# Kernel optimization log

Measured on AMD Instinct MI355X. Metric: run time of the kernel, lower is better.

The kernel has to match this reference:

```python
import jax, jax.numpy as jnp
import numpy as np
import math

TOPK = 13
NUM_CLASSES = 80
ALPHA = 1.0
BETA = 6.0
EPS = 1e-9


def ciou_xyxy(box1, box2, eps=1e-7):
    """CIoU between xyxy boxes; box1/box2 broadcastable [..., 4]. Returns [..., 1]."""
    b1x1, b1y1, b1x2, b1y2 = jnp.split(box1, 4, axis=-1)
    b2x1, b2y1, b2x2, b2y2 = jnp.split(box2, 4, axis=-1)
    w1, h1 = b1x2 - b1x1, b1y2 - b1y1 + eps
    w2, h2 = b2x2 - b2x1, b2y2 - b2y1 + eps
    inter = (jnp.minimum(b1x2, b2x2) - jnp.maximum(b1x1, b2x1)).clip(0) * \
            (jnp.minimum(b1y2, b2y2) - jnp.maximum(b1y1, b2y1)).clip(0)
    union = w1 * h1 + w2 * h2 - inter + eps
    iou = inter / union
    cw = jnp.maximum(b1x2, b2x2) - jnp.minimum(b1x1, b2x1)
    ch = jnp.maximum(b1y2, b2y2) - jnp.minimum(b1y1, b2y1)
    c2 = cw ** 2 + ch ** 2 + eps
    rho2 = ((b2x1 + b2x2 - b1x1 - b1x2) ** 2 + (b2y1 + b2y2 - b1y1 - b1y2) ** 2) / 4
    v = (4.0 / math.pi ** 2) * (jnp.arctan(w2 / h2) - jnp.arctan(w1 / h1)) ** 2
    alpha = jax.lax.stop_gradient(v / (v - iou + (1 + eps)))  # torch.no_grad block
    return iou - (rho2 / c2 + v * alpha)


def setup_inputs() -> dict:
    key = jax.random.key(0)
    ks = jax.random.split(key, 8)
    bs, M = 16, 64
    # YOLOv8 anchor grid: strides 8/16/32 on a 640x640 image -> 8400 points
    pts = []
    for s, n in ((8, 80), (16, 40), (32, 20)):
        xs = (np.arange(n, dtype=np.float32) + 0.5) * s
        gx, gy = np.meshgrid(xs, xs)
        pts.append(np.stack([gx.ravel(), gy.ravel()], -1))
    anc_points = jnp.asarray(np.concatenate(pts, 0), jnp.float32)  # (8400, 2)
    A = anc_points.shape[0]
    pd_scores = jax.random.uniform(ks[0], (bs, A, NUM_CLASSES), jnp.float32)
    c = jax.random.uniform(ks[1], (bs, A, 2), jnp.float32) * 640.0
    wh = jax.random.uniform(ks[2], (bs, A, 2), jnp.float32) * 120.0 + 8.0
    pd_bboxes = jnp.concatenate([c - wh / 2, c + wh / 2], -1)  # xyxy
    gc = jax.random.uniform(ks[3], (bs, M, 2), jnp.float32) * 560.0 + 40.0
    gwh = jax.random.uniform(ks[4], (bs, M, 2), jnp.float32) * 200.0 + 20.0
    gt_bboxes = jnp.concatenate([gc - gwh / 2, gc + gwh / 2], -1)
    gt_labels = jax.random.randint(ks[5], (bs, M, 1), 0, NUM_CLASSES, dtype=jnp.int32)
    mask_gt = (jax.random.uniform(ks[6], (bs, M, 1)) > 0.25).astype(jnp.float32)
    return {"pd_scores": pd_scores, "pd_bboxes": pd_bboxes, "anc_points": anc_points,
            "gt_labels": gt_labels, "gt_bboxes": gt_bboxes, "mask_gt": mask_gt}


def _assign(pd_scores, pd_bboxes, anc_points, gt_labels, gt_bboxes, mask_gt):
    bs, A, nc = pd_scores.shape
    M = gt_bboxes.shape[1]
    dt = pd_scores.dtype

    # ---- select_candidates_in_gts: anchors inside gt boxes -> (b, M, A) ----
    lt = gt_bboxes[:, :, None, :2]            # (b, M, 1, 2)
    rb = gt_bboxes[:, :, None, 2:]
    xy = anc_points[None, None]               # (1, 1, A, 2)
    deltas = jnp.concatenate([xy - lt, rb - xy], axis=-1)  # (b, M, A, 4)
    mask_in_gts = (deltas.min(-1) > EPS).astype(dt)        # (b, M, A)

    # ---- get_box_metrics ----
    bidx = jnp.arange(bs)[:, None]                         # (b, 1)
    labels = gt_labels[..., 0].astype(jnp.int32)           # (b, M)
    bbox_scores = pd_scores[bidx, :, labels]               # (b, M, A)
    overlaps = ciou_xyxy(gt_bboxes[:, :, None, :], pd_bboxes[:, None, :, :])
    overlaps = overlaps[..., 0].clip(0)                    # (b, M, A)
    align_metric = bbox_scores ** ALPHA * overlaps ** BETA

    # ---- select_topk_candidates (scatter-add instead of one_hot over 8400) ----
    metrics = align_metric * mask_in_gts
    _, topk_idxs = jax.lax.top_k(metrics, TOPK)            # (b, M, topk)
    valid = mask_gt > 0                                    # (b, M, 1) bool
    topk_idxs = jnp.where(valid, topk_idxs, 0)
    counts = jnp.zeros((bs, M, A), dt).at[
        jnp.arange(bs)[:, None, None], jnp.arange(M)[None, :, None], topk_idxs
    ].add(1.0)
    mask_topk = jnp.where(counts > 1, jnp.zeros((), dt), counts)
    mask_pos = mask_topk * mask_in_gts * mask_gt           # (b, M, A)

    # ---- select_highest_overlaps (unconditional; identity when no conflicts) ----
    fg_mask = mask_pos.sum(-2)                             # (b, A)
    mask_multi = fg_mask[:, None, :] > 1                   # (b, 1, A)
    max_idx = overlaps.argmax(1)                           # (b, A)
    is_max = jnp.swapaxes(jax.nn.one_hot(max_idx, M, dtype=dt), 1, 2)  # (b, M, A)
    mask_pos = jnp.where(mask_multi, is_max, mask_pos)
    fg_mask = mask_pos.sum(-2)
    target_gt_idx = mask_pos.argmax(-2)                    # (b, A)

    # ---- get_targets ----
    flat_idx = target_gt_idx + bidx * M                    # (b, A) into b*M
    target_labels = jnp.clip(gt_labels.reshape(-1)[flat_idx], 0)   # (b, A)
    target_bboxes = gt_bboxes.reshape(-1, 4)[flat_idx]             # (b, A, 4)
    target_scores = jax.nn.one_hot(target_labels, NUM_CLASSES, dtype=dt)
    target_scores = jnp.where(fg_mask[..., None] > 0, target_scores, jnp.zeros((), dt))

    # ---- normalize scores by aligned metric ----
    align_metric = align_metric * mask_pos
    pos_align = align_metric.max(-1, keepdims=True)        # (b, M, 1)
    pos_overlaps = (overlaps * mask_pos).max(-1, keepdims=True)
    norm = (align_metric * pos_overlaps / (pos_align + EPS)).max(-2)[..., None]  # (b, A, 1)
    target_scores = target_scores * norm

    return target_labels, target_bboxes, target_scores, fg_mask.astype(bool), target_gt_idx


def reference(pd_scores, pd_bboxes, anc_points, gt_labels, gt_bboxes, mask_gt):
    return _assign(pd_scores, pd_bboxes, anc_points, gt_labels, gt_bboxes, mask_gt)
```

## Files before the change

kernel.cpp:

```cpp
#include <hip/hip_runtime.h>

#define A_TOT 8400
#define NCLS  80
#define MGT   64
#define TK    13
#define EPS7  1e-7f
#define EPS9  1e-9f
#define INV_PI2 0.4052847345693511f

__device__ __forceinline__ float ciou_clip(
    float gx1, float gy1, float gx2, float gy2, float ga, float area1,
    float px1, float py1, float px2, float py2, float pa)
{
  float w2 = px2 - px1, h2 = py2 - py1 + EPS7;
  float iw = fmaxf(fminf(gx2, px2) - fmaxf(gx1, px1), 0.f);
  float ih = fmaxf(fminf(gy2, py2) - fmaxf(gy1, py1), 0.f);
  float inter = iw * ih;
  float uni = area1 + w2 * h2 - inter + EPS7;
  float iou = inter / uni;
  float cw = fmaxf(gx2, px2) - fminf(gx1, px1);
  float ch = fmaxf(gy2, py2) - fminf(gy1, py1);
  float c2 = cw * cw + ch * ch + EPS7;
  float dx = px1 + px2 - gx1 - gx2;
  float dy = py1 + py2 - gy1 - gy2;
  float rho2 = (dx * dx + dy * dy) * 0.25f;
  float dd = pa - ga;
  float v = INV_PI2 * dd * dd;
  float alpha = v / (v - iou + (1.f + EPS7));
  float c = iou - (rho2 / c2 + v * alpha);
  return fmaxf(c, 0.f);
}

__device__ __forceinline__ unsigned long long wmax64(unsigned long long k) {
#pragma unroll
  for (int s = 32; s > 0; s >>= 1) {
    unsigned long long o = __shfl_xor(k, s, 64);
    k = (o > k) ? o : k;
  }
  return k;
}

__global__ void k_pre(const float* __restrict__ pd_bboxes,
                      const float* __restrict__ gt_bboxes,
                      float* __restrict__ patan, float* __restrict__ gatan,
                      int na, int nm)
{
  int t = blockIdx.x * 256 + threadIdx.x;
  if (t < na) {
    float4 bx = ((const float4*)pd_bboxes)[t];
    patan[t] = atanf((bx.z - bx.x) / (bx.w - bx.y + EPS7));
  } else if (t < na + nm) {
    int r = t - na;
    float4 bx = ((const float4*)gt_bboxes)[r];
    gatan[r] = atanf((bx.z - bx.x) / (bx.w - bx.y + EPS7));
  }
}

__global__ __launch_bounds__(64)
void k_topk(const float* __restrict__ pd_scores,
            const float* __restrict__ pd_bboxes,
            const float* __restrict__ anc,
            const int* __restrict__ gt_labels,
            const float* __restrict__ gt_bboxes,
            const float* __restrict__ mask_gt,
            const float* __restrict__ patan,
            const float* __restrict__ gatan,
            unsigned long long* __restrict__ mask64)
{
  int row = blockIdx.x;
  if (mask_gt[row] <= 0.f) return;
  int b = row >> 6;
  int m = row & 63;
  int lane = threadIdx.x;

  float4 g = ((const float4*)gt_bboxes)[row];
  float ga = gatan[row];
  float area1 = (g.z - g.x) * (g.w - g.y + EPS7);
  int label = gt_labels[row];
  const float*  ps   = pd_scores + (size_t)b * A_TOT * NCLS + label;
  const float4* pb   = (const float4*)(pd_bboxes + (size_t)b * A_TOT * 4);
  const float*  pat  = patan + (size_t)b * A_TOT;
  const float2* anc2 = (const float2*)anc;

  unsigned long long l[TK];
#pragma unroll
  for (int k = 0; k < TK; ++k) l[k] = 0ULL;

  auto insert = [&](unsigned long long key) {
    if (key > l[TK - 1]) {
#pragma unroll
      for (int j = TK - 1; j > 0; --j) {
        unsigned long long prev = l[j - 1];
        l[j] = (key > prev) ? prev : ((key > l[j]) ? key : l[j]);
      }
      l[0] = (key > l[0]) ? key : l[0];
    }
  };
  auto metric_key = [&](int a, float ax, float ay) -> unsigned long long {
    float dmin = fminf(fminf(ax - g.x, ay - g.y), fminf(g.z - ax, g.w - ay));
    unsigned long long key = (unsigned long long)(~(unsigned)a);
    if (dmin > EPS9) {
      float4 p = pb[a];
      float ov = ciou_clip(g.x, g.y, g.z, g.w, ga, area1, p.x, p.y, p.z, p.w, pat[a]);
      float o2 = ov * ov;
      float metric = ps[(size_t)a * NCLS] * (o2 * o2 * o2);
      key |= ((unsigned long long)__float_as_uint(metric)) << 32;
    }
    return key;
  };

  {
    float2 an = anc2[lane];
    insert(metric_key(lane, an.x, an.y));
  }

  const int   ns[3] = {80, 40, 20};
  const float ss[3] = {8.f, 16.f, 32.f};
  const int   bb[3] = {0, 6400, 8000};
#pragma unroll
  for (int sc = 0; sc < 3; ++sc) {
    int n = ns[sc]; float s = ss[sc]; int base = bb[sc];
    float inv_s = 1.f / s;
    int xlo = max(0,     (int)floorf(g.x * inv_s - 0.5f));
    int xhi = min(n - 1, (int)ceilf (g.z * inv_s - 0.5f));
    int ylo = max(0,     (int)floorf(g.y * inv_s - 0.5f));
    int yhi = min(n - 1, (int)ceilf (g.w * inv_s - 0.5f));
    int nx = xhi - xlo + 1, ny = yhi - ylo + 1;
    if (nx <= 0 || ny <= 0) continue;
    int tot = nx * ny;
    float invnx = 1.f / (float)nx;
    for (int r = lane; r < tot; r += 64) {
      int q  = (int)floorf(((float)r + 0.5f) * invnx);
      int ix = xlo + (r - q * nx);
      int iy = ylo + q;
      int a = base + iy * n + ix;
      if (a < 64) continue;
      float ax = ((float)ix + 0.5f) * s;
      float ay = ((float)iy + 0.5f) * s;
      float dmin = fminf(fminf(ax - g.x, ay - g.y), fminf(g.z - ax, g.w - ay));
      if (dmin > EPS9) {
        float4 p = pb[a];
        float ov = ciou_clip(g.x, g.y, g.z, g.w, ga, area1, p.x, p.y, p.z, p.w, pat[a]);
        float o2 = ov * ov;
        float metric = ps[(size_t)a * NCLS] * (o2 * o2 * o2);
        insert((((unsigned long long)__float_as_uint(metric)) << 32) |
               (unsigned long long)(~(unsigned)a));
      }
    }
  }

  unsigned long long res = 0ULL;
#pragma unroll
  for (int r = 0; r < TK; ++r) {
    unsigned long long w = wmax64(l[0]);
    if (lane == r) res = w;
    if (l[0] == w) {
#pragma unroll
      for (int j = 0; j < TK - 1; ++j) l[j] = l[j + 1];
      l[TK - 1] = 0ULL;
    }
  }

  if (lane < TK) {
    unsigned a = ~(unsigned)res;
    float2 an = anc2[a];
    float dmin = fminf(fminf(an.x - g.x, an.y - g.y), fminf(g.z - an.x, g.w - an.y));
    if (dmin > EPS9)
      atomicOr(mask64 + (size_t)b * A_TOT + a, 1ULL << m);
  }
}

__global__ __launch_bounds__(256)
void k_resolve(const float* __restrict__ pd_scores,
               const float* __restrict__ pd_bboxes,
               const int* __restrict__ gt_labels,
               const float* __restrict__ gt_bboxes,
               const float* __restrict__ patan,
               const float* __restrict__ gatan,
               const unsigned long long* __restrict__ mask64,
               int* __restrict__ tgt_ws, float* __restrict__ am_ws,
               unsigned int* __restrict__ pos_al, unsigned int* __restrict__ pos_ov,
               int total)
{
  int t = blockIdx.x * 256 + threadIdx.x;
  bool valid = t < total;
  unsigned long long msk = valid ? mask64[t] : 0ULL;
  int pc = __popcll(msk);
  float4 p = make_float4(0.f, 0.f, 0.f, 0.f);
  float pa_own = 0.f;
  if (valid && pc >= 1) {
    p = ((const float4*)pd_bboxes)[t];
    pa_own = patan[t];
  }
  if (valid && pc == 0) tgt_ws[t] = -1;
  if (valid && pc == 1) {
    int b = t / A_TOT;
    int tgt = __ffsll(msk) - 1;
    int gi = b * MGT + tgt;
    float4 g = ((const float4*)gt_bboxes)[gi];
    float area1 = (g.z - g.x) * (g.w - g.y + EPS7);
    float ov = ciou_clip(g.x, g.y, g.z, g.w, gatan[gi], area1,
                         p.x, p.y, p.z, p.w, pa_own);
    int label = gt_labels[gi];
    float sc = pd_scores[(size_t)t * NCLS + label];
    float o2 = ov * ov;
    float am = sc * (o2 * o2 * o2);
    tgt_ws[t] = tgt; am_ws[t] = am;
    atomicMax(pos_al + gi, __float_as_uint(am));
    atomicMax(pos_ov + gi, __float_as_uint(ov));
  }
  unsigned long long mb = __ballot(valid && pc > 1);
  int lane = threadIdx.x & 63;
  while (mb) {
    int src = __ffsll(mb) - 1; mb &= mb - 1;
    int   tt  = __shfl(t, src);
    float px1 = __shfl(p.x, src), py1 = __shfl(p.y, src);
    float px2 = __shfl(p.z, src), py2 = __shfl(p.w, src);
    float pa  = __shfl(pa_own, src);
    int bb2 = tt / A_TOT;
    int gi = bb2 * MGT + lane;
    float4 g = ((const float4*)gt_bboxes)[gi];
    float area1 = (g.z - g.x) * (g.w - g.y + EPS7);
    float ov = ciou_clip(g.x, g.y, g.z, g.w, gatan[gi], area1,
                         px1, py1, px2, py2, pa);
    unsigned long long key =
        (((unsigned long long)__float_as_uint(ov)) << 6) | (unsigned)(63 - lane);
    unsigned long long w = wmax64(key);
    if (key == w) {
      int label = gt_labels[gi];
      float sc = pd_scores[(size_t)tt * NCLS + label];
      float o2 = ov * ov;
      float am = sc * (o2 * o2 * o2);
      tgt_ws[tt] = lane; am_ws[tt] = am;
      atomicMax(pos_al + gi, __float_as_uint(am));
      atomicMax(pos_ov + gi, __float_as_uint(ov));
    }
  }
}

__global__ __launch_bounds__(256)
void k_write(const int* __restrict__ tgt_ws, const float* __restrict__ am_ws,
             const unsigned int* __restrict__ pos_al,
             const unsigned int* __restrict__ pos_ov,
             const int* __restrict__ gt_labels, const float* __restrict__ gt_bboxes,
             float* __restrict__ out, int bs)
{
  __shared__ int   slab[256];
  __shared__ float snorm[256];
  int total = bs * A_TOT;
  int base = blockIdx.x * 256;
  int t = base + threadIdx.x;
  int nrows = total - base; if (nrows > 256) nrows = 256;
  size_t OFF_BOX = (size_t)total;
  size_t OFF_SCR = OFF_BOX + (size_t)total * 4;
  size_t OFF_FG  = OFF_SCR + (size_t)total * NCLS;
  size_t OFF_TGT = OFF_FG + (size_t)total;
  if (t < total) {
    int b = t / A_TOT;
    int tw = tgt_ws[t];
    bool fg = tw >= 0;
    int tgt = fg ? tw : 0;
    int gi = b * MGT + tgt;
    int lab = gt_labels[gi]; if (lab < 0) lab = 0;
    float4 box = ((const float4*)gt_bboxes)[gi];
    float nrm = 0.f;
    if (fg) {
      float pa_ = __uint_as_float(pos_al[gi]);
      float po  = __uint_as_float(pos_ov[gi]);
      nrm = am_ws[t] * po / (pa_ + EPS9);
    }
    out[t] = (float)lab;
    ((float4*)(out + OFF_BOX))[t] = box;
    out[OFF_FG + t]  = fg ? 1.f : 0.f;
    out[OFF_TGT + t] = (float)tgt;
    slab[threadIdx.x]  = lab;
    snorm[threadIdx.x] = nrm;
  }
  __syncthreads();
  float4* srow = (float4*)(out + OFF_SCR + (size_t)base * NCLS);
  int nvec = nrows * (NCLS / 4);
  for (int u = threadIdx.x; u < nvec; u += 256) {
    int i  = u / (NCLS / 4);
    int c0 = (u - i * (NCLS / 4)) * 4;
    int lb = slab[i]; float nv = snorm[i];
    float4 v;
    v.x = (lb == c0    ) ? nv : 0.f;
    v.y = (lb == c0 + 1) ? nv : 0.f;
    v.z = (lb == c0 + 2) ? nv : 0.f;
    v.w = (lb == c0 + 3) ? nv : 0.f;
    srow[u] = v;
  }
}

extern "C" void kernel_launch(void* const* d_in, const int* in_sizes, int n_in,
                              void* d_out, int out_size, void* d_ws, size_t ws_size,
                              hipStream_t stream)
{
  const float* pd_scores = (const float*)d_in[0];
  const float* pd_bboxes = (const float*)d_in[1];
  const float* anc       = (const float*)d_in[2];
  const int*   gt_labels = (const int*)d_in[3];
  const float* gt_bboxes = (const float*)d_in[4];
  const float* mask_gt   = (const float*)d_in[5];
  int bs = in_sizes[0] / (A_TOT * NCLS);
  int NA = bs * A_TOT, NM = bs * MGT;

  unsigned long long* mask64 = (unsigned long long*)d_ws;
  unsigned int* pos_al = (unsigned int*)(mask64 + NA);
  unsigned int* pos_ov = pos_al + NM;
  int*   tgt_ws = (int*)(pos_ov + NM);
  float* am_ws  = (float*)(tgt_ws + NA);
  float* patan  = am_ws + NA;
  float* gatan  = patan + NA;

  hipMemsetAsync(mask64, 0, (size_t)NA * 8 + (size_t)NM * 8, stream);

  k_pre<<<(NA + NM + 255) / 256, 256, 0, stream>>>(pd_bboxes, gt_bboxes,
                                                   patan, gatan, NA, NM);
  k_topk<<<NM, 64, 0, stream>>>(pd_scores, pd_bboxes, anc, gt_labels, gt_bboxes,
                                mask_gt, patan, gatan, mask64);
  k_resolve<<<(NA + 255) / 256, 256, 0, stream>>>(pd_scores, pd_bboxes, gt_labels,
                                                  gt_bboxes, patan, gatan, mask64,
                                                  tgt_ws, am_ws, pos_al, pos_ov, NA);
  k_write<<<(NA + 255) / 256, 256, 0, stream>>>(tgt_ws, am_ws, pos_al, pos_ov,
                                                gt_labels, gt_bboxes, (float*)d_out, bs);
}
```

Baseline: 132.7 us.

## Widen top-k blocks to four wavefronts and compute atan inline, dropping pre-pass

The per-GT top-k kernel now runs 256 threads (four wavefronts) instead of one. Each wavefront keeps its own per-lane top-13 lists, and the four candidate sets are merged through shared memory by the first wavefront. The separate atan precompute kernel is removed; aspect-ratio arctangents are computed inline where needed, saving one launch and its global traffic at the cost of extra transcendental work per evaluated anchor. The first 256 anchors are always inserted, which keeps the index-tiebreak semantics of the original.

```diff
diff --git a/kernel.cpp b/kernel.cpp
--- a/kernel.cpp
+++ b/kernel.cpp
@@ -4,6 +4,7 @@
 #define NCLS  80
 #define MGT   64
 #define TK    13
+#define NT    256
 #define EPS7  1e-7f
 #define EPS9  1e-9f
 #define INV_PI2 0.4052847345693511f
@@ -40,46 +41,27 @@
   return k;
 }
 
-__global__ void k_pre(const float* __restrict__ pd_bboxes,
-                      const float* __restrict__ gt_bboxes,
-                      float* __restrict__ patan, float* __restrict__ gatan,
-                      int na, int nm)
-{
-  int t = blockIdx.x * 256 + threadIdx.x;
-  if (t < na) {
-    float4 bx = ((const float4*)pd_bboxes)[t];
-    patan[t] = atanf((bx.z - bx.x) / (bx.w - bx.y + EPS7));
-  } else if (t < na + nm) {
-    int r = t - na;
-    float4 bx = ((const float4*)gt_bboxes)[r];
-    gatan[r] = atanf((bx.z - bx.x) / (bx.w - bx.y + EPS7));
-  }
-}
-
-__global__ __launch_bounds__(64)
+__global__ __launch_bounds__(NT)
 void k_topk(const float* __restrict__ pd_scores,
             const float* __restrict__ pd_bboxes,
             const float* __restrict__ anc,
             const int* __restrict__ gt_labels,
             const float* __restrict__ gt_bboxes,
             const float* __restrict__ mask_gt,
-            const float* __restrict__ patan,
-            const float* __restrict__ gatan,
             unsigned long long* __restrict__ mask64)
 {
   int row = blockIdx.x;
   if (mask_gt[row] <= 0.f) return;
   int b = row >> 6;
   int m = row & 63;
-  int lane = threadIdx.x;
+  int tid = threadIdx.x, lane = tid & 63, wid = tid >> 6;
 
   float4 g = ((const float4*)gt_bboxes)[row];
-  float ga = gatan[row];
+  float ga = atanf((g.z - g.x) / (g.w - g.y + EPS7));
   float area1 = (g.z - g.x) * (g.w - g.y + EPS7);
   int label = gt_labels[row];
   const float*  ps   = pd_scores + (size_t)b * A_TOT * NCLS + label;
   const float4* pb   = (const float4*)(pd_bboxes + (size_t)b * A_TOT * 4);
-  const float*  pat  = patan + (size_t)b * A_TOT;
   const float2* anc2 = (const float2*)anc;
 
   unsigned long long l[TK];
@@ -96,22 +78,23 @@
       l[0] = (key > l[0]) ? key : l[0];
     }
   };
-  auto metric_key = [&](int a, float ax, float ay) -> unsigned long long {
-    float dmin = fminf(fminf(ax - g.x, ay - g.y), fminf(g.z - ax, g.w - ay));
+  auto eval_inbox = [&](int a) -> unsigned long long {
+    float4 p = pb[a];
+    float pa = atanf((p.z - p.x) / (p.w - p.y + EPS7));
+    float ov = ciou_clip(g.x, g.y, g.z, g.w, ga, area1, p.x, p.y, p.z, p.w, pa);
+    float o2 = ov * ov;
+    float metric = ps[(size_t)a * NCLS] * (o2 * o2 * o2);
+    return (((unsigned long long)__float_as_uint(metric)) << 32) |
+           (unsigned long long)(~(unsigned)a);
+  };
+
+  {
+    int a = tid;
+    float2 an = anc2[a];
+    float dmin = fminf(fminf(an.x - g.x, an.y - g.y), fminf(g.z - an.x, g.w - an.y));
     unsigned long long key = (unsigned long long)(~(unsigned)a);
-    if (dmin > EPS9) {
-      float4 p = pb[a];
-      float ov = ciou_clip(g.x, g.y, g.z, g.w, ga, area1, p.x, p.y, p.z, p.w, pat[a]);
-      float o2 = ov * ov;
-      float metric = ps[(size_t)a * NCLS] * (o2 * o2 * o2);
-      key |= ((unsigned long long)__float_as_uint(metric)) << 32;
-    }
-    return key;
-  };
-
-  {
-    float2 an = anc2[lane];
-    insert(metric_key(lane, an.x, an.y));
+    if (dmin > EPS9) key = eval_inbox(a);
+    insert(key);
   }
 
   const int   ns[3] = {80, 40, 20};
@@ -129,44 +112,50 @@
     if (nx <= 0 || ny <= 0) continue;
     int tot = nx * ny;
     float invnx = 1.f / (float)nx;
-    for (int r = lane; r < tot; r += 64) {
+    for (int r = tid; r < tot; r += NT) {
       int q  = (int)floorf(((float)r + 0.5f) * invnx);
       int ix = xlo + (r - q * nx);
       int iy = ylo + q;
       int a = base + iy * n + ix;
-      if (a < 64) continue;
+      if (a < NT) continue;
       float ax = ((float)ix + 0.5f) * s;
       float ay = ((float)iy + 0.5f) * s;
       float dmin = fminf(fminf(ax - g.x, ay - g.y), fminf(g.z - ax, g.w - ay));
-      if (dmin > EPS9) {
-        float4 p = pb[a];
-        float ov = ciou_clip(g.x, g.y, g.z, g.w, ga, area1, p.x, p.y, p.z, p.w, pat[a]);
-        float o2 = ov * ov;
-        float metric = ps[(size_t)a * NCLS] * (o2 * o2 * o2);
-        insert((((unsigned long long)__float_as_uint(metric)) << 32) |
-               (unsigned long long)(~(unsigned)a));
-      }
-    }
-  }
-
-  unsigned long long res = 0ULL;
+      if (dmin > EPS9) insert(eval_inbox(a));
+    }
+  }
+
+  __shared__ unsigned long long sk[4 * TK];
+  unsigned long long wres = 0ULL;
 #pragma unroll
   for (int r = 0; r < TK; ++r) {
     unsigned long long w = wmax64(l[0]);
-    if (lane == r) res = w;
+    if (lane == r) wres = w;
     if (l[0] == w) {
 #pragma unroll
       for (int j = 0; j < TK - 1; ++j) l[j] = l[j + 1];
       l[TK - 1] = 0ULL;
     }
   }
-
-  if (lane < TK) {
-    unsigned a = ~(unsigned)res;
-    float2 an = anc2[a];
-    float dmin = fminf(fminf(an.x - g.x, an.y - g.y), fminf(g.z - an.x, g.w - an.y));
-    if (dmin > EPS9)
-      atomicOr(mask64 + (size_t)b * A_TOT + a, 1ULL << m);
+  if (lane < TK) sk[wid * TK + lane] = wres;
+  __syncthreads();
+
+  if (wid == 0) {
+    unsigned long long c = (lane < 4 * TK) ? sk[lane] : 0ULL;
+    unsigned long long res = 0ULL;
+#pragma unroll
+    for (int r = 0; r < TK; ++r) {
+      unsigned long long w = wmax64(c);
+      if (lane == r) res = w;
+      if (c == w) c = 0ULL;
+    }
+    if (lane < TK) {
+      unsigned a = ~(unsigned)res;
+      float2 an = anc2[a];
+      float dmin = fminf(fminf(an.x - g.x, an.y - g.y), fminf(g.z - an.x, g.w - an.y));
+      if (dmin > EPS9)
+        atomicOr(mask64 + (size_t)b * A_TOT + a, 1ULL << m);
+    }
   }
 }
 
@@ -175,8 +164,6 @@
                const float* __restrict__ pd_bboxes,
                const int* __restrict__ gt_labels,
                const float* __restrict__ gt_bboxes,
-               const float* __restrict__ patan,
-               const float* __restrict__ gatan,
                const unsigned long long* __restrict__ mask64,
                int* __restrict__ tgt_ws, float* __restrict__ am_ws,
                unsigned int* __restrict__ pos_al, unsigned int* __restrict__ pos_ov,
@@ -190,7 +177,7 @@
   float pa_own = 0.f;
   if (valid && pc >= 1) {
     p = ((const float4*)pd_bboxes)[t];
-    pa_own = patan[t];
+    pa_own = atanf((p.z - p.x) / (p.w - p.y + EPS7));
   }
   if (valid && pc == 0) tgt_ws[t] = -1;
   if (valid && pc == 1) {
@@ -198,8 +185,9 @@
     int tgt = __ffsll(msk) - 1;
     int gi = b * MGT + tgt;
     float4 g = ((const float4*)gt_bboxes)[gi];
+    float ga = atanf((g.z - g.x) / (g.w - g.y + EPS7));
     float area1 = (g.z - g.x) * (g.w - g.y + EPS7);
-    float ov = ciou_clip(g.x, g.y, g.z, g.w, gatan[gi], area1,
+    float ov = ciou_clip(g.x, g.y, g.z, g.w, ga, area1,
                          p.x, p.y, p.z, p.w, pa_own);
     int label = gt_labels[gi];
     float sc = pd_scores[(size_t)t * NCLS + label];
@@ -220,8 +208,9 @@
     int bb2 = tt / A_TOT;
     int gi = bb2 * MGT + lane;
     float4 g = ((const float4*)gt_bboxes)[gi];
+    float ga = atanf((g.z - g.x) / (g.w - g.y + EPS7));
     float area1 = (g.z - g.x) * (g.w - g.y + EPS7);
-    float ov = ciou_clip(g.x, g.y, g.z, g.w, gatan[gi], area1,
+    float ov = ciou_clip(g.x, g.y, g.z, g.w, ga, area1,
                          px1, py1, px2, py2, pa);
     unsigned long long key =
         (((unsigned long long)__float_as_uint(ov)) << 6) | (unsigned)(63 - lane);
@@ -310,17 +299,13 @@
   unsigned int* pos_ov = pos_al + NM;
   int*   tgt_ws = (int*)(pos_ov + NM);
   float* am_ws  = (float*)(tgt_ws + NA);
-  float* patan  = am_ws + NA;
-  float* gatan  = patan + NA;
 
   hipMemsetAsync(mask64, 0, (size_t)NA * 8 + (size_t)NM * 8, stream);
 
-  k_pre<<<(NA + NM + 255) / 256, 256, 0, stream>>>(pd_bboxes, gt_bboxes,
-                                                   patan, gatan, NA, NM);
-  k_topk<<<NM, 64, 0, stream>>>(pd_scores, pd_bboxes, anc, gt_labels, gt_bboxes,
-                                mask_gt, patan, gatan, mask64);
+  k_topk<<<NM, NT, 0, stream>>>(pd_scores, pd_bboxes, anc, gt_labels, gt_bboxes,
+                                mask_gt, mask64);
   k_resolve<<<(NA + 255) / 256, 256, 0, stream>>>(pd_scores, pd_bboxes, gt_labels,
-                                                  gt_bboxes, patan, gatan, mask64,
+                                                  gt_bboxes, mask64,
                                                   tgt_ws, am_ws, pos_al, pos_ov, NA);
   k_write<<<(NA + 255) / 256, 256, 0, stream>>>(tgt_ws, am_ws, pos_al, pos_ov,
                                                 gt_labels, gt_bboxes, (float*)d_out, bs);
```

Result: faster. 128.7 us (-3.0%).
